# Performance work log

Measured on AMD Instinct MI355X. Metric: run time of the kernel, lower is better.

## Reference

```python
import jax, jax.numpy as jnp
import numpy as np


def _conv(x, w, b, stride=1):
    # NCHW conv, 3x3 kernel, padding=1
    y = jax.lax.conv_general_dilated(
        x, w, (stride, stride), [(1, 1), (1, 1)],
        dimension_numbers=("NCHW", "OIHW", "NCHW"))
    return y + b[None, :, None, None]


def setup_inputs() -> dict:
    key = jax.random.key(0)
    ks = jax.random.split(key, 13)
    s = 0.05
    d = jnp.float32
    return {
        "x": jax.random.normal(ks[0], (1, 3, 512, 512), d),
        "low0_w": jax.random.normal(ks[1], (64, 3, 3, 3), d) * s,
        "low0_b": jax.random.normal(ks[2], (64,), d) * s,
        "ll_rh_w": jax.random.normal(ks[3], (4, 61, 61, 3, 3), d) * s,
        "ll_rh_b": jax.random.normal(ks[4], (4, 61), d) * s,
        "ll_lh_w": jax.random.normal(ks[5], (4, 3, 3, 3, 3), d) * s,
        "ll_lh_b": jax.random.normal(ks[6], (4, 3), d) * s,
        "hl0_w": jax.random.normal(ks[7], (64, 61, 3, 3), d) * s,
        "hl0_b": jax.random.normal(ks[8], (64,), d) * s,
        "hl_w": jax.random.normal(ks[9], (3, 64, 64, 3, 3), d) * s,
        "hl_b": jax.random.normal(ks[10], (3, 64), d) * s,
        "lin_w": jax.random.normal(ks[11], (30, 64), d) * s,
        "lin_b": jax.random.normal(ks[12], (30,), d) * s,
    }


def reference(x, low0_w, low0_b, ll_rh_w, ll_rh_b, ll_lh_w, ll_lh_b,
              hl0_w, hl0_b, hl_w, hl_b, lin_w, lin_b):
    # ---- low-level path: 64-channel full-resolution features ----
    I = _conv(x, low0_w, low0_b)  # (b,64,H,W)
    for i in range(ll_rh_w.shape[0]):
        rh = jax.nn.relu(_conv(I[:, :61], ll_rh_w[i], ll_rh_b[i]))
        lh = jnp.tanh(_conv(I[:, 61:], ll_lh_w[i], ll_lh_b[i]))
        I = jnp.concatenate([rh, lh], axis=1)
    # ---- high-level path: predicts 30 params -> 3x10 color transform ----
    h = _conv(I[:, :61], hl0_w, hl0_b)
    for i in range(hl_w.shape[0]):
        h = jax.nn.relu(_conv(h, hl_w[i], hl_b[i], stride=2))
        h = jax.lax.reduce_window(h, -jnp.inf, jax.lax.max,
                                  (1, 1, 2, 2), (1, 1, 2, 2), "VALID")
    g = h.mean(axis=(2, 3))            # (b,64) global average pool
    Wp = g @ lin_w.T + lin_b           # (b,30)
    Wm = Wp.reshape(3, 10)             # batch=1, matches torch reshape
    # ---- vectorized Tform: per-pixel quadratic feature expansion ----
    I3 = I[:, 61:]                     # (b,3,H,W)
    r, gc, bc = I3[:, 0], I3[:, 1], I3[:, 2]
    feats = jnp.stack([r * r, r * gc, r * bc, r,
                       gc * gc, gc * bc, gc,
                       bc * bc, bc, jnp.ones_like(r)], axis=1)  # (b,10,H,W)
    return jnp.einsum("ok,bkhw->bohw", Wm, feats)  # (b,3,H,W)
```

## Files before the change

### kernel.cpp

```cpp
#include <hip/hip_runtime.h>
#include <cstdint>

typedef _Float16 half8 __attribute__((ext_vector_type(8)));
typedef float f32x4 __attribute__((ext_vector_type(4)));

#define HW_ (512*512)

__global__ __launch_bounds__(256)
void pre_k(const float* __restrict__ x, const float* __restrict__ low0_w,
           const float* __restrict__ low0_b,
           const float* __restrict__ rh_w, const float* __restrict__ hl0_w,
           const float* __restrict__ hl_w, _Float16* __restrict__ M,
           float* __restrict__ L, _Float16* __restrict__ wt,
           _Float16* __restrict__ zg)
{
    __shared__ float tile[3 * 324];
    if (blockIdx.x < 144) {
        if (blockIdx.x == 0 && threadIdx.x < 32) zg[threadIdx.x] = (_Float16)0.f;
        int t = blockIdx.x * 256 + threadIdx.x;
        if (t >= 8 * 4608) return;
        int layer = t / 4608;
        int r = t - layer * 4608;
        int lane = r & 63, ci = r >> 6;
        int m = ci & 3, kk = (ci >> 2) & 1, s = ci >> 3;
        int o = m * 16 + (lane & 15);
        int cb = kk * 32 + ((lane >> 4) & 3) * 8;
        const float* w; int O, CIN;
        if (layer < 4)      { w = rh_w + (size_t)layer * 61 * 61 * 9; O = 61; CIN = 61; }
        else if (layer == 4){ w = hl0_w;                              O = 64; CIN = 61; }
        else                { w = hl_w + (size_t)(layer - 5) * 64 * 64 * 9; O = 64; CIN = 64; }
        half8 v;
        #pragma unroll
        for (int j = 0; j < 8; ++j) {
            int c = cb + j;
            float f = (o < O && c < CIN) ? w[((size_t)o * CIN + c) * 9 + s] : 0.f;
            v[j] = (_Float16)f;
        }
        *(half8*)(wt + (size_t)layer * 36864 + (size_t)r * 8) = v;
        return;
    }

    const int id = blockIdx.x - 144;
    const int bx = id & 31, by = (id >> 5) & 31, z = id >> 10;
    const int tx = threadIdx.x & 15, ty = threadIdx.x >> 4;
    const int ox = bx * 16 + tx, oy = by * 16 + ty;
    const int ix0 = bx * 16 - 1, iy0 = by * 16 - 1;

    for (int i = threadIdx.x; i < 3 * 324; i += 256) {
        int c = i / 324, p = i - c * 324;
        int iy = p / 18, ix = p - iy * 18;
        int gy = iy0 + iy, gx = ix0 + ix;
        float v = 0.f;
        if ((unsigned)gy < 512u && (unsigned)gx < 512u)
            v = x[(size_t)c * HW_ + (size_t)gy * 512 + gx];
        tile[i] = v;
    }
    __syncthreads();

    float p9[3][9];
    #pragma unroll
    for (int c = 0; c < 3; ++c)
        #pragma unroll
        for (int dy = 0; dy < 3; ++dy)
            #pragma unroll
            for (int dx = 0; dx < 3; ++dx)
                p9[c][dy * 3 + dx] = tile[c * 324 + (ty + dy) * 18 + tx + dx];

    float acc[16];
    #pragma unroll
    for (int o = 0; o < 16; ++o) {
        int oc = z * 16 + o;
        float a = low0_b[oc];
        const float* wo = low0_w + (size_t)oc * 27;
        #pragma unroll
        for (int c = 0; c < 3; ++c)
            #pragma unroll
            for (int k = 0; k < 9; ++k)
                a = fmaf(p9[c][k], wo[c * 9 + k], a);
        acc[o] = a;
    }

    const size_t pix = (size_t)oy * 512 + ox;
    half8 h0, h1;
    #pragma unroll
    for (int o = 0; o < 8; ++o) { h0[o] = (_Float16)acc[o]; h1[o] = (_Float16)acc[8 + o]; }
    _Float16* orow = M + pix * 64 + z * 16;
    *(half8*)(orow)     = h0;
    *(half8*)(orow + 8) = h1;
    if (z == 3) {
        #pragma unroll
        for (int o = 13; o < 16; ++o)
            L[(size_t)(o - 13) * HW_ + pix] = acc[o];
    }
}

template<int O, int ACT, int DOLH>
__global__ __launch_bounds__(256, 2)
void conv_mfma_k(const _Float16* __restrict__ in, const _Float16* __restrict__ wt,
                 const float* __restrict__ bias, _Float16* __restrict__ out,
                 const float* __restrict__ L_in, const float* __restrict__ lhw,
                 const float* __restrict__ lhb, float* __restrict__ L_out,
                 const _Float16* __restrict__ zg)
{
    __shared__ _Float16 __attribute__((aligned(16))) in_t[2592 * 8];
    __shared__ _Float16 __attribute__((aligned(16))) wbuf[2][8192];
    const int tid = threadIdx.x;
    const int l = tid & 63, wv = tid >> 6;
    const int px = l & 15, g = l >> 4;
    const int orig = blockIdx.x;
    const int id = ((orig & 7) << 7) + (orig >> 3);
    const int bx = id & 31, by = id >> 5;
    const int iy0 = by * 16 - 1, ix0 = bx * 16 - 1;

    #pragma unroll
    for (int k = 0; k < 11; ++k) {
        int i = tid + (k << 8);
        if (i < 2592) {
            int p = i >> 3, jl = i & 7;
            int iy = p / 18, ix = p - iy * 18;
            int gy = iy0 + iy, gx = ix0 + ix;
            int j = jl ^ (p & 7);
            const _Float16* src = ((unsigned)gy < 512u && (unsigned)gx < 512u)
                ? in + ((size_t)gy * 512 + gx) * 64 + j * 8 : zg;
            __builtin_amdgcn_global_load_lds(
                (const __attribute__((address_space(1))) void*)src,
                (__attribute__((address_space(3))) void*)(in_t + (size_t)(i - l) * 8),
                16, 0, 0);
        }
    }
    #pragma unroll
    for (int it = 0; it < 4; ++it) {
        int ci = (it << 8) + tid;
        __builtin_amdgcn_global_load_lds(
            (const __attribute__((address_space(1))) void*)(wt + ci * 8),
            (__attribute__((address_space(3))) void*)(wbuf[0] + (size_t)(ci - l) * 8),
            16, 0, 0);
    }
    __syncthreads();

    float bs[4][4];
    #pragma unroll
    for (int m = 0; m < 4; ++m)
        #pragma unroll
        for (int r = 0; r < 4; ++r) {
            int o = m * 16 + g * 4 + r;
            bs[m][r] = (o < O) ? bias[o] : 0.f;
        }

    f32x4 acc[4][4];
    #pragma unroll
    for (int m = 0; m < 4; ++m)
        #pragma unroll
        for (int f = 0; f < 4; ++f) acc[m][f] = (f32x4){0.f, 0.f, 0.f, 0.f};

    #pragma unroll
    for (int ph = 0; ph < 5; ++ph) {
        if (ph < 3) {
            #pragma unroll
            for (int it = 0; it < 4; ++it) {
                int ci = (it << 8) + tid;
                __builtin_amdgcn_global_load_lds(
                    (const __attribute__((address_space(1))) void*)(wt + (size_t)(ph + 1) * 8192 + ci * 8),
                    (__attribute__((address_space(3))) void*)(wbuf[(ph + 1) & 1] + (size_t)(ci - l) * 8),
                    16, 0, 0);
            }
        } else if (ph == 3) {
            #pragma unroll
            for (int it = 0; it < 2; ++it) {
                int ci = (it << 8) + tid;
                __builtin_amdgcn_global_load_lds(
                    (const __attribute__((address_space(1))) void*)(wt + (size_t)8 * 4096 + ci * 8),
                    (__attribute__((address_space(3))) void*)(wbuf[0] + (size_t)(ci - l) * 8),
                    16, 0, 0);
            }
        }
        const int ntap = (ph < 4) ? 2 : 1;
        const _Float16* wbb = wbuf[ph & 1];
        #pragma unroll
        for (int tl = 0; tl < ntap; ++tl) {
            const int s = 2 * ph + tl;
            const _Float16* wb = wbb + (tl << 12);
            half8 a[8];
            #pragma unroll
            for (int q = 0; q < 8; ++q)
                a[q] = *(const half8*)(wb + (q << 9) + l * 8);

            const int dy = s / 3, dx = s - dy * 3;
            #pragma unroll
            for (int f = 0; f < 4; ++f) {
                int ipix = (4 * wv + f + dy) * 18 + px + dx;
                int rb = ipix * 64, sw = (ipix & 7) << 3;
                #pragma unroll
                for (int kk = 0; kk < 2; ++kk) {
                    half8 b = *(const half8*)&in_t[rb + ((kk * 32 + g * 8) ^ sw)];
                    #pragma unroll
                    for (int m = 0; m < 4; ++m)
                        acc[m][f] = __builtin_amdgcn_mfma_f32_16x16x32_f16(
                            a[kk * 4 + m], b, acc[m][f], 0, 0, 0);
                }
            }
        }
        __syncthreads();
    }

    #pragma unroll
    for (int f = 0; f < 4; ++f) {
        const int p = (4 * wv + f) * 16 + px;
        const int sw = p & 7;
        #pragma unroll
        for (int m = 0; m < 4; ++m) {
            union { _Float16 h[4]; uint2 u; } pk;
            #pragma unroll
            for (int r = 0; r < 4; ++r) {
                int o = m * 16 + g * 4 + r;
                float v = acc[m][f][r] + bs[m][r];
                if (ACT) v = fmaxf(v, 0.f);
                pk.h[r] = (o < O) ? (_Float16)v : (_Float16)0.f;
            }
            int chunk = (m * 2 + (g >> 1)) ^ sw;
            *(uint2*)&in_t[p * 64 + chunk * 8 + (g & 1) * 4] = pk.u;
        }
    }
    __syncthreads();
    #pragma unroll
    for (int k = 0; k < 8; ++k) {
        int q = (k << 8) + tid;
        int p = q >> 3, jc = q & 7;
        half8 v = *(const half8*)&in_t[p * 64 + ((jc ^ (p & 7)) * 8)];
        int row = p >> 4, col = p & 15;
        _Float16* dst = out + (((size_t)(by * 16 + row) * 512) + bx * 16 + col) * 64 + jc * 8;
        *(half8*)dst = v;
    }

    if (DOLH) {
        const int tx = tid & 15, ty = tid >> 4;
        const int oy = by * 16 + ty, ox = bx * 16 + tx;
        float pv[27];
        #pragma unroll
        for (int c = 0; c < 3; ++c)
            #pragma unroll
            for (int d2 = 0; d2 < 9; ++d2) {
                int gy = oy + d2 / 3 - 1, gx = ox + d2 % 3 - 1;
                pv[c * 9 + d2] = ((unsigned)gy < 512u && (unsigned)gx < 512u)
                    ? L_in[(size_t)c * HW_ + (size_t)gy * 512 + gx] : 0.f;
            }
        const size_t pix = (size_t)oy * 512 + ox;
        #pragma unroll
        for (int oc = 0; oc < 3; ++oc) {
            float a = lhb[oc];
            #pragma unroll
            for (int k = 0; k < 27; ++k)
                a = fmaf(pv[k], lhw[oc * 27 + k], a);
            L_out[(size_t)oc * HW_ + pix] = tanhf(a);
        }
    }
}

template<int FP32OUT, int NB>
__global__ __launch_bounds__(256, 3)
void conv_s2_pool_k(const _Float16* __restrict__ in, int Hin,
                    const _Float16* __restrict__ wt,
                    const float* __restrict__ bias, void* __restrict__ outv,
                    const _Float16* __restrict__ zg)
{
    const int Hp = Hin >> 2;
    __shared__ _Float16 __attribute__((aligned(16))) in_t[2312 * 8];
    __shared__ _Float16 __attribute__((aligned(16))) wbuf[2][4096];
    const int tid = threadIdx.x;
    const int l = tid & 63, wv = tid >> 6;
    const int n = l & 15, g = l >> 4;
    int id = blockIdx.x;
    if (NB == 32) id = ((id & 7) << 7) + (id >> 3);
    const int bx = id % NB, by = id / NB;
    const int iy0 = by * 16 - 1, ix0 = bx * 16 - 1;

    #pragma unroll
    for (int k = 0; k < 10; ++k) {
        int i = tid + (k << 8);
        if (i < 2312) {
            int p = i >> 3, jl = i & 7;
            int iy = p / 17, ix = p - iy * 17;
            int gy = iy0 + iy, gx = ix0 + ix;
            int j = jl ^ (p & 7);
            const _Float16* src =
                ((unsigned)gy < (unsigned)Hin && (unsigned)gx < (unsigned)Hin)
                    ? in + ((size_t)gy * Hin + gx) * 64 + j * 8 : zg;
            __builtin_amdgcn_global_load_lds(
                (const __attribute__((address_space(1))) void*)src,
                (__attribute__((address_space(3))) void*)(in_t + (size_t)(i - l) * 8),
                16, 0, 0);
        }
    }
    #pragma unroll
    for (int it = 0; it < 2; ++it) {
        int ci = (it << 8) + tid;
        __builtin_amdgcn_global_load_lds(
            (const __attribute__((address_space(1))) void*)(wt + ci * 8),
            (__attribute__((address_space(3))) void*)(wbuf[0] + (size_t)(ci - l) * 8),
            16, 0, 0);
    }
    __syncthreads();

    float bs[4];
    #pragma unroll
    for (int r = 0; r < 4; ++r) bs[r] = bias[wv * 16 + g * 4 + r];

    f32x4 acc[4];
    #pragma unroll
    for (int f = 0; f < 4; ++f) acc[f] = (f32x4){0.f, 0.f, 0.f, 0.f};

    const int py_lo = n >> 3, pxc = n & 7;
    #pragma unroll
    for (int s = 0; s < 9; ++s) {
        if (s < 8) {
            #pragma unroll
            for (int it = 0; it < 2; ++it) {
                int ci = (it << 8) + tid;
                __builtin_amdgcn_global_load_lds(
                    (const __attribute__((address_space(1))) void*)(wt + ((s + 1) << 12) + ci * 8),
                    (__attribute__((address_space(3))) void*)(wbuf[(s + 1) & 1] + (size_t)(ci - l) * 8),
                    16, 0, 0);
            }
        }
        const _Float16* wb = wbuf[s & 1];
        half8 a[2];
        #pragma unroll
        for (int kk = 0; kk < 2; ++kk)
            a[kk] = *(const half8*)(wb + ((kk * 4 + wv) << 9) + l * 8);

        const int dy = s / 3, dx = s - dy * 3;
        #pragma unroll
        for (int f = 0; f < 4; ++f) {
            int py = 2 * f + py_lo;
            int ipix = (2 * py + dy) * 17 + 2 * pxc + dx;
            int rb = ipix * 64, sw = (ipix & 7) << 3;
            #pragma unroll
            for (int kk = 0; kk < 2; ++kk) {
                half8 b = *(const half8*)&in_t[rb + ((kk * 32 + g * 8) ^ sw)];
                acc[f] = __builtin_amdgcn_mfma_f32_16x16x32_f16(a[kk], b, acc[f], 0, 0, 0);
            }
        }
        __syncthreads();
    }

    #pragma unroll
    for (int f = 0; f < 4; ++f)
        #pragma unroll
        for (int r = 0; r < 4; ++r) {
            float v = fmaxf(acc[f][r] + bs[r], 0.f);
            v = fmaxf(v, __shfl_xor(v, 1));
            v = fmaxf(v, __shfl_xor(v, 8));
            if ((l & 9) == 0) {
                int o = wv * 16 + g * 4 + r;
                size_t pp = ((size_t)(by * 4 + f) * Hp + bx * 4 + (n >> 1)) * 64 + o;
                if (FP32OUT) ((float*)outv)[pp] = v;
                else         ((_Float16*)outv)[pp] = (_Float16)v;
            }
        }
}

__global__ void meanlin_k(const float* __restrict__ h,
                          const float* __restrict__ lw,
                          const float* __restrict__ lb,
                          float* __restrict__ wm)
{
    __shared__ float g[64];
    int t = threadIdx.x;
    if (t < 64) {
        float s = 0.f;
        for (int p = 0; p < 64; ++p) s += h[p * 64 + t];
        g[t] = s * (1.f / 64.f);
    }
    __syncthreads();
    if (t < 30) {
        float s = lb[t];
        for (int c = 0; c < 64; ++c) s = fmaf(g[c], lw[t * 64 + c], s);
        wm[t] = s;
    }
}

__global__ __launch_bounds__(256)
void final_k(const float* __restrict__ I3, const float* __restrict__ wm,
             float* __restrict__ out)
{
    __shared__ float W[30];
    if (threadIdx.x < 30) W[threadIdx.x] = wm[threadIdx.x];
    __syncthreads();
    const int HW = 512 * 512;
    for (int i = blockIdx.x * blockDim.x + threadIdx.x; i < HW;
         i += gridDim.x * blockDim.x) {
        float r = I3[i], g = I3[HW + i], b = I3[2 * HW + i];
        float f[10] = { r * r, r * g, r * b, r, g * g, g * b, g, b * b, b, 1.f };
        #pragma unroll
        for (int o = 0; o < 3; ++o) {
            float s = 0.f;
            #pragma unroll
            for (int k = 0; k < 10; ++k) s = fmaf(W[o * 10 + k], f[k], s);
            out[(size_t)o * HW + i] = s;
        }
    }
}

extern "C" void kernel_launch(void* const* d_in, const int* in_sizes, int n_in,
                              void* d_out, int out_size, void* d_ws, size_t ws_size,
                              hipStream_t stream)
{
    const float* x      = (const float*)d_in[0];
    const float* low0_w = (const float*)d_in[1];
    const float* low0_b = (const float*)d_in[2];
    const float* rh_w   = (const float*)d_in[3];
    const float* rh_b   = (const float*)d_in[4];
    const float* lh_w   = (const float*)d_in[5];
    const float* lh_b   = (const float*)d_in[6];
    const float* hl0_w  = (const float*)d_in[7];
    const float* hl0_b  = (const float*)d_in[8];
    const float* hl_w   = (const float*)d_in[9];
    const float* hl_b   = (const float*)d_in[10];
    const float* lin_w  = (const float*)d_in[11];
    const float* lin_b  = (const float*)d_in[12];
    float* out = (float*)d_out;

    const size_t HW = 512 * 512;
    _Float16* M0 = (_Float16*)d_ws;
    _Float16* M1 = M0 + (size_t)64 * HW;
    _Float16* P0 = M1 + (size_t)64 * HW;
    _Float16* P1 = P0 + (size_t)16384 * 64;
    _Float16* WT = P1 + (size_t)1024 * 64;
    _Float16* ZG = WT + (size_t)8 * 36864;
    float*    P2 = (float*)(ZG + 32);
    float*    L0 = P2 + 64 * 64;
    float*    L1 = L0 + (size_t)3 * HW;
    float*    WM = L1 + (size_t)3 * HW;

    dim3 blk(256);

    pre_k<<<dim3(4240), blk, 0, stream>>>(x, low0_w, low0_b,
                                          rh_w, hl0_w, hl_w, M0, L0, WT, ZG);

    _Float16* cur = M0; _Float16* nxt = M1;
    float* Lc = L0; float* Ln = L1;
    for (int i = 0; i < 4; ++i) {
        conv_mfma_k<61, 1, 1><<<dim3(1024), blk, 0, stream>>>(
            cur, WT + (size_t)i * 36864, rh_b + i * 61, nxt,
            Lc, lh_w + (size_t)i * 81, lh_b + i * 3, Ln, ZG);
        _Float16* t = cur; cur = nxt; nxt = t;
        float* tl = Lc; Lc = Ln; Ln = tl;
    }

    conv_mfma_k<64, 0, 0><<<dim3(1024), blk, 0, stream>>>(
        cur, WT + (size_t)4 * 36864, hl0_b, nxt,
        nullptr, nullptr, nullptr, nullptr, ZG);

    conv_s2_pool_k<0, 32><<<dim3(1024), blk, 0, stream>>>(
        nxt, 512, WT + (size_t)5 * 36864, hl_b, (void*)P0, ZG);
    conv_s2_pool_k<0, 8><<<dim3(64), blk, 0, stream>>>(
        P0, 128, WT + (size_t)6 * 36864, hl_b + 64, (void*)P1, ZG);
    conv_s2_pool_k<1, 2><<<dim3(4), blk, 0, stream>>>(
        P1, 32, WT + (size_t)7 * 36864, hl_b + 128, (void*)P2, ZG);

    meanlin_k<<<dim3(1), dim3(64), 0, stream>>>(P2, lin_w, lin_b, WM);

    final_k<<<dim3(2048), blk, 0, stream>>>(Lc, WM, out);
}
```

Baseline: 208.5 us.

## Triple-buffer per-tap weight loads in conv and fuse mean/linear into final kernel

The MFMA conv kernel now streams weights one tap at a time into a three-slot LDS ring, replacing the earlier two-tap double buffer. Each step waits with a partial vmcnt and then a raw s_barrier, so loads can stay in flight across iterations, at the cost of nine barriers instead of five. LDS use for weights falls, which may help occupancy. Separately, the global mean and linear layer are folded into every block of final_k, removing one kernel launch while each block redundantly recomputes the 30 parameters.

```diff
diff --git a/kernel.cpp b/kernel.cpp
--- a/kernel.cpp
+++ b/kernel.cpp
@@ -103,7 +103,7 @@
                  const _Float16* __restrict__ zg)
 {
     __shared__ _Float16 __attribute__((aligned(16))) in_t[2592 * 8];
-    __shared__ _Float16 __attribute__((aligned(16))) wbuf[2][8192];
+    __shared__ _Float16 __attribute__((aligned(16))) wbuf[3][4096];
     const int tid = threadIdx.x;
     const int l = tid & 63, wv = tid >> 6;
     const int px = l & 15, g = l >> 4;
@@ -129,12 +129,15 @@
         }
     }
     #pragma unroll
-    for (int it = 0; it < 4; ++it) {
-        int ci = (it << 8) + tid;
-        __builtin_amdgcn_global_load_lds(
-            (const __attribute__((address_space(1))) void*)(wt + ci * 8),
-            (__attribute__((address_space(3))) void*)(wbuf[0] + (size_t)(ci - l) * 8),
-            16, 0, 0);
+    for (int tp = 0; tp < 2; ++tp) {
+        #pragma unroll
+        for (int it = 0; it < 2; ++it) {
+            int ci = (it << 8) + tid;
+            __builtin_amdgcn_global_load_lds(
+                (const __attribute__((address_space(1))) void*)(wt + (size_t)tp * 4096 + ci * 8),
+                (__attribute__((address_space(3))) void*)(wbuf[tp] + (size_t)(ci - l) * 8),
+                16, 0, 0);
+        }
     }
     __syncthreads();
 
@@ -154,53 +157,42 @@
         for (int f = 0; f < 4; ++f) acc[m][f] = (f32x4){0.f, 0.f, 0.f, 0.f};
 
     #pragma unroll
-    for (int ph = 0; ph < 5; ++ph) {
-        if (ph < 3) {
-            #pragma unroll
-            for (int it = 0; it < 4; ++it) {
-                int ci = (it << 8) + tid;
-                __builtin_amdgcn_global_load_lds(
-                    (const __attribute__((address_space(1))) void*)(wt + (size_t)(ph + 1) * 8192 + ci * 8),
-                    (__attribute__((address_space(3))) void*)(wbuf[(ph + 1) & 1] + (size_t)(ci - l) * 8),
-                    16, 0, 0);
-            }
-        } else if (ph == 3) {
+    for (int s = 0; s < 9; ++s) {
+        if (s < 7) {
             #pragma unroll
             for (int it = 0; it < 2; ++it) {
                 int ci = (it << 8) + tid;
                 __builtin_amdgcn_global_load_lds(
-                    (const __attribute__((address_space(1))) void*)(wt + (size_t)8 * 4096 + ci * 8),
-                    (__attribute__((address_space(3))) void*)(wbuf[0] + (size_t)(ci - l) * 8),
+                    (const __attribute__((address_space(1))) void*)(wt + (size_t)(s + 2) * 4096 + ci * 8),
+                    (__attribute__((address_space(3))) void*)(wbuf[(s + 2) % 3] + (size_t)(ci - l) * 8),
                     16, 0, 0);
             }
         }
-        const int ntap = (ph < 4) ? 2 : 1;
-        const _Float16* wbb = wbuf[ph & 1];
-        #pragma unroll
-        for (int tl = 0; tl < ntap; ++tl) {
-            const int s = 2 * ph + tl;
-            const _Float16* wb = wbb + (tl << 12);
-            half8 a[8];
-            #pragma unroll
-            for (int q = 0; q < 8; ++q)
-                a[q] = *(const half8*)(wb + (q << 9) + l * 8);
-
-            const int dy = s / 3, dx = s - dy * 3;
-            #pragma unroll
-            for (int f = 0; f < 4; ++f) {
-                int ipix = (4 * wv + f + dy) * 18 + px + dx;
-                int rb = ipix * 64, sw = (ipix & 7) << 3;
+        const _Float16* wb = wbuf[s % 3];
+        half8 a[8];
+        #pragma unroll
+        for (int q = 0; q < 8; ++q)
+            a[q] = *(const half8*)(wb + (q << 9) + l * 8);
+
+        const int dy = s / 3, dx = s - dy * 3;
+        #pragma unroll
+        for (int f = 0; f < 4; ++f) {
+            int ipix = (4 * wv + f + dy) * 18 + px + dx;
+            int rb = ipix * 64, sw = (ipix & 7) << 3;
+            #pragma unroll
+            for (int kk = 0; kk < 2; ++kk) {
+                half8 b = *(const half8*)&in_t[rb + ((kk * 32 + g * 8) ^ sw)];
                 #pragma unroll
-                for (int kk = 0; kk < 2; ++kk) {
-                    half8 b = *(const half8*)&in_t[rb + ((kk * 32 + g * 8) ^ sw)];
-                    #pragma unroll
-                    for (int m = 0; m < 4; ++m)
-                        acc[m][f] = __builtin_amdgcn_mfma_f32_16x16x32_f16(
-                            a[kk * 4 + m], b, acc[m][f], 0, 0, 0);
-                }
-            }
-        }
-        __syncthreads();
+                for (int m = 0; m < 4; ++m)
+                    acc[m][f] = __builtin_amdgcn_mfma_f32_16x16x32_f16(
+                        a[kk * 4 + m], b, acc[m][f], 0, 0, 0);
+            }
+        }
+        __builtin_amdgcn_sched_barrier(0);
+        if (s < 7) asm volatile("s_waitcnt vmcnt(2)" ::: "memory");
+        else       asm volatile("s_waitcnt vmcnt(0)" ::: "memory");
+        __builtin_amdgcn_s_barrier();
+        asm volatile("" ::: "memory");
     }
 
     #pragma unroll
@@ -359,38 +351,41 @@
         }
 }
 
-__global__ void meanlin_k(const float* __restrict__ h,
-                          const float* __restrict__ lw,
-                          const float* __restrict__ lb,
-                          float* __restrict__ wm)
+__global__ __launch_bounds__(256)
+void final_k(const float* __restrict__ P2, const float* __restrict__ lw,
+             const float* __restrict__ lb, const float* __restrict__ I3,
+             float* __restrict__ out)
 {
+    __shared__ float part[256];
     __shared__ float g[64];
-    int t = threadIdx.x;
-    if (t < 64) {
+    __shared__ float W[30];
+    const int t = threadIdx.x;
+    {
+        int c = t >> 2, q = t & 3;
         float s = 0.f;
-        for (int p = 0; p < 64; ++p) s += h[p * 64 + t];
-        g[t] = s * (1.f / 64.f);
-    }
+        #pragma unroll
+        for (int k = 0; k < 16; ++k)
+            s += P2[(q * 16 + k) * 64 + c];
+        part[t] = s;
+    }
+    __syncthreads();
+    if (t < 64)
+        g[t] = (part[t * 4] + part[t * 4 + 1] + part[t * 4 + 2] + part[t * 4 + 3])
+               * (1.f / 64.f);
     __syncthreads();
     if (t < 30) {
         float s = lb[t];
+        #pragma unroll
         for (int c = 0; c < 64; ++c) s = fmaf(g[c], lw[t * 64 + c], s);
-        wm[t] = s;
-    }
-}
-
-__global__ __launch_bounds__(256)
-void final_k(const float* __restrict__ I3, const float* __restrict__ wm,
-             float* __restrict__ out)
-{
-    __shared__ float W[30];
-    if (threadIdx.x < 30) W[threadIdx.x] = wm[threadIdx.x];
-    __syncthreads();
+        W[t] = s;
+    }
+    __syncthreads();
+
     const int HW = 512 * 512;
-    for (int i = blockIdx.x * blockDim.x + threadIdx.x; i < HW;
+    for (int i = blockIdx.x * blockDim.x + t; i < HW;
          i += gridDim.x * blockDim.x) {
-        float r = I3[i], g = I3[HW + i], b = I3[2 * HW + i];
-        float f[10] = { r * r, r * g, r * b, r, g * g, g * b, g, b * b, b, 1.f };
+        float r = I3[i], gc = I3[HW + i], b = I3[2 * HW + i];
+        float f[10] = { r * r, r * gc, r * b, r, gc * gc, gc * b, gc, b * b, b, 1.f };
         #pragma unroll
         for (int o = 0; o < 3; ++o) {
             float s = 0.f;
@@ -430,7 +425,6 @@
     float*    P2 = (float*)(ZG + 32);
     float*    L0 = P2 + 64 * 64;
     float*    L1 = L0 + (size_t)3 * HW;
-    float*    WM = L1 + (size_t)3 * HW;
 
     dim3 blk(256);
 
@@ -458,7 +452,5 @@
     conv_s2_pool_k<1, 2><<<dim3(4), blk, 0, stream>>>(
         P1, 32, WT + (size_t)7 * 36864, hl_b + 128, (void*)P2, ZG);
 
-    meanlin_k<<<dim3(1), dim3(64), 0, stream>>>(P2, lin_w, lin_b, WM);
-
-    final_k<<<dim3(2048), blk, 0, stream>>>(Lc, WM, out);
+    final_k<<<dim3(2048), blk, 0, stream>>>(P2, lin_w, lin_b, Lc, out);
 }
```

Measured after the change: 210.0 us. Within noise of the previous version (+0.7%).
